# Kernel tuning notes

Measured on AMD Instinct MI355X. Metric: run time of the kernel, lower is better.

The kernel has to match this reference:

```python
import jax, jax.numpy as jnp
import numpy as np

B, S, D = 1, 2048, 4096
HQ, HK, HD = 32, 8, 128


def setup_inputs() -> dict:
    key = jax.random.key(0)
    ks = jax.random.split(key, 6)
    x = jax.random.normal(ks[0], (B, S, D), jnp.float32) * 0.02
    wq = jax.random.normal(ks[1], (D, HQ * HD), jnp.float32) * 0.02
    wk = jax.random.normal(ks[2], (D, HK * HD), jnp.float32) * 0.02
    wv = jax.random.normal(ks[3], (D, HK * HD), jnp.float32) * 0.02
    wo = jax.random.normal(ks[4], (HQ * HD, D), jnp.float32) * 0.02
    # canonical RoPE frequencies: theta = 10000
    inv_freq = 1.0 / (10000.0 ** (jnp.arange(0, HD, 2, dtype=jnp.float32) / HD))  # [HD/2]
    t = jnp.arange(S, dtype=jnp.float32)
    ang = jnp.outer(t, inv_freq)  # [S, HD/2]
    return {
        "x": x,
        "freqs_cos": jnp.cos(ang),
        "freqs_sin": jnp.sin(ang),
        "wq": wq, "wk": wk, "wv": wv, "wo": wo,
    }


def _rope(t, cos, sin):
    # t: [B, S, H, HD]; pairs are consecutive elements (view_as_complex semantics)
    tr = t.reshape(*t.shape[:-1], HD // 2, 2)
    t0, t1 = tr[..., 0], tr[..., 1]
    c = cos[None, :, None, :]
    s = sin[None, :, None, :]
    o0 = t0 * c - t1 * s
    o1 = t0 * s + t1 * c
    return jnp.stack([o0, o1], axis=-1).reshape(t.shape)


def reference(x, freqs_cos, freqs_sin, wq, wk, wv, wo):
    b, s, _ = x.shape
    g = HQ // HK  # GQA group size
    xq = (x @ wq).reshape(b, s, HQ, HD)
    xk = (x @ wk).reshape(b, s, HK, HD)
    xv = (x @ wv).reshape(b, s, HK, HD)
    xq = _rope(xq, freqs_cos, freqs_sin)
    xk = _rope(xk, freqs_cos, freqs_sin)
    scale = 1.0 / jnp.sqrt(jnp.float32(HD))
    xqg = xq.reshape(b, s, HK, g, HD)
    # scores: [b, HK, g, s_q, s_k]
    scores = jnp.einsum("bqkgd,bnkd->bkgqn", xqg, xk) * scale
    causal = jnp.tril(jnp.ones((s, s), dtype=bool))
    scores = jnp.where(causal[None, None, None, :, :], scores, -jnp.inf)
    p = jax.nn.softmax(scores, axis=-1)
    out = jnp.einsum("bkgqn,bnkd->bqkgd", p, xv).reshape(b, s, HQ * HD)
    return out @ wo
```

## Files before the change

### kernel.cpp

```cpp
#include <hip/hip_runtime.h>
#include <stdint.h>

typedef __bf16 bf16_t;
typedef bf16_t bf16x8 __attribute__((ext_vector_type(8)));
typedef float f32x4 __attribute__((ext_vector_type(4)));
typedef unsigned int u32;
typedef unsigned short u16;

#define DEV_INLINE __device__ __forceinline__

#define S_LEN 2048
#define D_MODEL 4096
#define HQ 32
#define HK 8
#define HD 128
#define NQKV 6144

DEV_INLINE u16 f2bf(float x) {
  union { float f; uint32_t u; } v; v.f = x;
  uint32_t r = v.u + 0x7FFFu + ((v.u >> 16) & 1u);
  return (u16)(r >> 16);
}
DEV_INLINE float bf2f(u16 x) {
  union { uint32_t u; float f; } v; v.u = ((uint32_t)x) << 16;
  return v.f;
}
DEV_INLINE u32 pack2bf(float a, float b) {
  return (u32)f2bf(a) | ((u32)f2bf(b) << 16);
}

DEV_INLINE void async_load16(const void* g, void* l) {
  __builtin_amdgcn_global_load_lds(
      (const __attribute__((address_space(1))) u32*)g,
      (__attribute__((address_space(3))) u32*)l, 16, 0, 0);
}

DEV_INLINE f32x4 mfma16(bf16x8 a, bf16x8 b, f32x4 c) {
  return __builtin_amdgcn_mfma_f32_16x16x32_bf16(a, b, c, 0, 0, 0);
}

__global__ void cvt_f32_bf16(const float* __restrict__ in, u16* __restrict__ out, int n) {
  int i = (blockIdx.x * blockDim.x + threadIdx.x) * 4;
  if (i >= n) return;
  float4 v = *(const float4*)(in + i);
  union { u16 s[4]; uint2 u; } o;
  o.s[0] = f2bf(v.x); o.s[1] = f2bf(v.y); o.s[2] = f2bf(v.z); o.s[3] = f2bf(v.w);
  *(uint2*)(out + i) = o.u;
}

__global__ void transpose_f32_bf16(const float* __restrict__ in, u16* __restrict__ out,
                                   int R, int C) {
  __shared__ float tile[32][33];
  int tx = threadIdx.x, ty = threadIdx.y;
  int c0 = blockIdx.x * 32, r0 = blockIdx.y * 32;
#pragma unroll
  for (int i = 0; i < 4; ++i)
    tile[ty + i * 8][tx] = in[(long)(r0 + ty + i * 8) * C + c0 + tx];
  __syncthreads();
#pragma unroll
  for (int i = 0; i < 4; ++i)
    out[(long)(c0 + ty + i * 8) * R + r0 + tx] = f2bf(tile[tx][ty + i * 8]);
}

__global__ void transpose_bf16(const u16* __restrict__ in, u16* __restrict__ out,
                               int R, int C, int ld_in, int col_off) {
  __shared__ u16 tile[32][33];
  int tx = threadIdx.x, ty = threadIdx.y;
  int c0 = blockIdx.x * 32, r0 = blockIdx.y * 32;
#pragma unroll
  for (int i = 0; i < 4; ++i)
    tile[ty + i * 8][tx] = in[(long)(r0 + ty + i * 8) * ld_in + col_off + c0 + tx];
  __syncthreads();
#pragma unroll
  for (int i = 0; i < 4; ++i)
    out[(long)(c0 + ty + i * 8) * R + r0 + tx] = tile[tx][ty + i * 8];
}

__global__ void rope_bf16(const u16* __restrict__ in, const float* __restrict__ cosb,
                          const float* __restrict__ sinb, u16* __restrict__ out,
                          int H, int ld_in, int col_off, float scale) {
  int idx = blockIdx.x * blockDim.x + threadIdx.x;
  int j = idx & 63;
  int sh = idx >> 6;
  int s = sh / H, h = sh - s * H;
  const u16* ip = in + (long)s * ld_in + col_off + h * HD;
  union { u32 u; u16 s2[2]; } v; v.u = *(const u32*)(ip + 2 * j);
  float q0 = bf2f(v.s2[0]), q1 = bf2f(v.s2[1]);
  float c = cosb[s * 64 + j], sn = sinb[s * 64 + j];
  union { u16 s2[2]; u32 u; } o;
  o.s2[0] = f2bf((q0 * c - q1 * sn) * scale);
  o.s2[1] = f2bf((q0 * sn + q1 * c) * scale);
  *(u32*)(out + (long)sh * HD + 2 * j) = o.u;
}

#define BARRIER() asm volatile("s_barrier" ::: "memory")
#define WAIT_VM(N) asm volatile("s_waitcnt vmcnt(" #N ")" ::: "memory")

#define K_TILE(T, DO_STAGE, VMWAIT)                                               \
  {                                                                               \
    const u16* Ab_ = &lds[(T) & 3][0];                                            \
    const u16* Bb_ = &lds[(T) & 3][8192];                                         \
    bf16x8 bfr_[NF];                                                              \
    _Pragma("unroll")                                                             \
    for (int j = 0; j < NF; ++j) bfr_[j] = rdfrag(Bb_, wc * WCOLS + j * 16 + l15);\
    bf16x8 af0_[MFH];                                                             \
    _Pragma("unroll")                                                             \
    for (int i = 0; i < MFH; ++i) af0_[i] = rdfrag(Ab_, wr * MROWS + i * 16 + l15);\
    if (DO_STAGE) stageA((T) + 3);                                                \
    __builtin_amdgcn_s_setprio(1);                                                \
    _Pragma("unroll")                                                             \
    for (int i = 0; i < MFH; ++i)                                                 \
      _Pragma("unroll")                                                           \
      for (int j = 0; j < NF; ++j) acc[i][j] = mfma16(af0_[i], bfr_[j], acc[i][j]);\
    __builtin_amdgcn_s_setprio(0);                                                \
    bf16x8 af1_[MFH];                                                             \
    _Pragma("unroll")                                                             \
    for (int i = 0; i < MFH; ++i)                                                 \
      af1_[i] = rdfrag(Ab_, wr * MROWS + (MFH + i) * 16 + l15);                   \
    if (DO_STAGE) stageB((T) + 3);                                                \
    __builtin_amdgcn_s_setprio(1);                                                \
    _Pragma("unroll")                                                             \
    for (int i = 0; i < MFH; ++i)                                                 \
      _Pragma("unroll")                                                           \
      for (int j = 0; j < NF; ++j)                                                \
        acc[MFH + i][j] = mfma16(af1_[i], bfr_[j], acc[MFH + i][j]);              \
    __builtin_amdgcn_s_setprio(0);                                                \
    VMWAIT;                                                                       \
    BARRIER();                                                                    \
  }

template <int BN, int WM, bool BF16OUT>
__global__ __launch_bounds__(512, 2) void gemm_pipe(
    const u16* __restrict__ A, const u16* __restrict__ Bt, void* __restrict__ Cv,
    int N, int K) {
  constexpr int WN = 8 / WM;
  constexpr int MROWS = 256 / WM;
  constexpr int MF = MROWS / 16;
  constexpr int MFH = MF / 2;
  constexpr int NF = BN / (WN * 16);
  constexpr int WCOLS = NF * 16;
  constexpr int BCH = BN * 4;
  constexpr int BISS = (BCH + 511) / 512;
  constexpr int LDSU = (256 + BN) * 32;

  __shared__ __attribute__((aligned(16))) u16 lds[4][LDSU];

  const int tid = threadIdx.x;
  const int lane = tid & 63;
  const int wave = tid >> 6;
  const int quad = lane >> 4, l15 = lane & 15;
  const int wr = wave / WN, wc = wave % WN;

  const int gx = gridDim.x;
  const int bid = blockIdx.y * gx + blockIdx.x;
  const int cpx = (gx * gridDim.y) >> 3;
  const int sw = (bid & 7) * cpx + (bid >> 3);
  const int bn = sw % gx, bm = sw / gx;

  const long arow = (long)bm * 256, brow = (long)bn * BN;
  const int NT = K >> 5;

  auto stageA = [&](int ts) {
    const int bs = ts & 3;
    const int k0 = ts * 32;
#pragma unroll
    for (int j = 0; j < 2; ++j) {
      int c = tid + j * 512;
      int row = c >> 2, cc = c & 3, cs = cc ^ ((row >> 1) & 3);
      async_load16(A + (arow + row) * (long)K + k0 + cs * 8,
                   (u16*)&lds[bs][0] + c * 8);
    }
  };
  auto stageB = [&](int ts) {
    const int bs = ts & 3;
    const int k0 = ts * 32;
#pragma unroll
    for (int j = 0; j < BISS; ++j) {
      int c = tid + j * 512;
      int cd = (c < BCH) ? c : c - 256;
      int row = cd >> 2, cc = cd & 3, cs = cc ^ ((row >> 1) & 3);
      async_load16(Bt + (brow + row) * (long)K + k0 + cs * 8,
                   (u16*)&lds[bs][8192] + cd * 8);
    }
  };
  auto rdfrag = [&](const u16* base, int row) -> bf16x8 {
    return *(const bf16x8*)(base + row * 32 + ((quad ^ ((row >> 1) & 3)) * 8));
  };

  f32x4 acc[MF][NF] = {};

  stageA(0); stageB(0); stageA(1); stageB(1); stageA(2); stageB(2);
  if constexpr (BISS == 2) { WAIT_VM(8); } else { WAIT_VM(6); }
  BARRIER();

  int t = 0;
  for (; t < NT - 3; ++t) {
    if constexpr (BISS == 2) { K_TILE(t, true, WAIT_VM(8)); }
    else                     { K_TILE(t, true, WAIT_VM(6)); }
  }
  if constexpr (BISS == 2) { K_TILE(t, false, WAIT_VM(4)); }
  else                     { K_TILE(t, false, WAIT_VM(3)); }
  ++t;
  K_TILE(t, false, WAIT_VM(0));
  ++t;
  K_TILE(t, false, ((void)0));

#pragma unroll
  for (int i = 0; i < MF; ++i) {
    const long row = (long)bm * 256 + wr * MROWS + i * 16 + quad * 4;
#pragma unroll
    for (int j = 0; j < NF; ++j) {
      const int col = bn * BN + wc * WCOLS + j * 16 + l15;
      if constexpr (BF16OUT) {
        u16* C = (u16*)Cv;
#pragma unroll
        for (int r = 0; r < 4; ++r) C[(row + r) * N + col] = f2bf(acc[i][j][r]);
      } else {
        float* C = (float*)Cv;
#pragma unroll
        for (int r = 0; r < 4; ++r) C[(row + r) * N + col] = acc[i][j][r];
      }
    }
  }
}

#define NEG_INF -1e30f
__global__ __launch_bounds__(256, 2) void attn_fwd(
    const u16* __restrict__ Qb, const u16* __restrict__ Kb,
    const u16* __restrict__ Vt, u16* __restrict__ Ob) {
  __shared__ __attribute__((aligned(16))) u16 Ks[2][64 * 128];
  __shared__ __attribute__((aligned(16))) u16 Vs[2][128 * 64];
  __shared__ __attribute__((aligned(16))) u16 Pts[4][16 * 64];
  const int tid = threadIdx.x;
  const int lane = tid & 63, wave = tid >> 6;
  const int quad = lane >> 4, l15 = lane & 15;
  const int lin = blockIdx.y * gridDim.x + blockIdx.x;
  const int h = lin & 31;
  const int pp = (lin >> 5) & 7;
  const int u = (lin >> 8) ? 15 - pp : pp;
  const int hk = h >> 2;
  const int swz = 2 * (l15 & 7);
  const int nt = 2 * (u + 1);

  bf16x8 qf[2][4];
#pragma unroll
  for (int n = 0; n < 2; ++n) {
    const u16* qrow = Qb + (long)(u * 128 + wave * 32 + n * 16 + l15) * (HQ * HD)
                      + h * HD + quad * 8;
#pragma unroll
    for (int ks = 0; ks < 4; ++ks) qf[n][ks] = *(const bf16x8*)(qrow + ks * 32);
  }

  auto stage = [&](int t) {
    const int b = t & 1;
#pragma unroll
    for (int it = 0; it < 4; ++it) {
      int c = tid + it * 256;
      int row = c >> 4, cc = c & 15, cs = cc ^ (row & 15);
      async_load16(Kb + (long)(t * 64 + row) * (HK * HD) + hk * HD + cs * 8,
                   (u16*)&Ks[b][0] + c * 8);
    }
#pragma unroll
    for (int it = 0; it < 4; ++it) {
      int c = tid + it * 256;
      int row = c >> 3, cc = c & 7, cs = cc ^ (row & 7);
      async_load16(Vt + (long)(hk * HD + row) * S_LEN + t * 64 + cs * 8,
                   (u16*)&Vs[b][0] + c * 8);
    }
  };

  float m_run[2] = {NEG_INF, NEG_INF}, l_run[2] = {0.f, 0.f};
  f32x4 oacc[8][2] = {};

  stage(0);
  __syncthreads();

  for (int t = 0; t < nt; ++t) {
    const int cur = t & 1;
    if (t + 1 < nt) stage(t + 1);

    if (t * 64 <= u * 128 + wave * 32 + 31) {
      f32x4 sc[4][2] = {};
      __builtin_amdgcn_s_setprio(1);
#pragma unroll
      for (int ks = 0; ks < 4; ++ks)
#pragma unroll
        for (int tj = 0; tj < 4; ++tj) {
          int row = tj * 16 + l15;
          bf16x8 kf = *(const bf16x8*)(&Ks[cur][0] + row * 128
                                       + (((ks * 4 + quad) ^ (row & 15)) * 8));
          sc[tj][0] = mfma16(kf, qf[0][ks], sc[tj][0]);
          sc[tj][1] = mfma16(kf, qf[1][ks], sc[tj][1]);
        }
      __builtin_amdgcn_s_setprio(0);

      const bool diag = (t >= 2 * u);
      const int kbase = t * 64 - u * 128;
#pragma unroll
      for (int n = 0; n < 2; ++n) {
        int qloc = wave * 32 + n * 16 + l15;
        if (diag) {
#pragma unroll
          for (int tj = 0; tj < 4; ++tj)
#pragma unroll
            for (int r = 0; r < 4; ++r)
              if (kbase + tj * 16 + quad * 4 + r > qloc) sc[tj][n][r] = NEG_INF;
        }
        float m = NEG_INF;
#pragma unroll
        for (int tj = 0; tj < 4; ++tj)
#pragma unroll
          for (int r = 0; r < 4; ++r) m = fmaxf(m, sc[tj][n][r]);
        m = fmaxf(m, __shfl_xor(m, 16));
        m = fmaxf(m, __shfl_xor(m, 32));
        if (!__all(m - m_run[n] <= 8.0f)) {
          float mnew = fmaxf(m_run[n], m);
          float alpha = __expf(m_run[n] - mnew);
          m_run[n] = mnew;
          l_run[n] *= alpha;
#pragma unroll
          for (int tj = 0; tj < 8; ++tj) oacc[tj][n] *= alpha;
        }
        float rs = 0.f;
#pragma unroll
        for (int tj = 0; tj < 4; ++tj)
#pragma unroll
          for (int r = 0; r < 4; ++r) {
            float p = __expf(sc[tj][n][r] - m_run[n]);
            sc[tj][n][r] = p;
            rs += p;
          }
        rs += __shfl_xor(rs, 16);
        rs += __shfl_xor(rs, 32);
        l_run[n] += rs;
      }

      u16* pw = &Pts[wave][0];
      bf16x8 pf0[2], pf1[2];
#pragma unroll
      for (int tj = 0; tj < 4; ++tj) {
        union { u32 w[2]; uint2 u2; } pk;
        pk.w[0] = pack2bf(sc[tj][0][0], sc[tj][0][1]);
        pk.w[1] = pack2bf(sc[tj][0][2], sc[tj][0][3]);
        *(uint2*)(pw + l15 * 64 + (((tj * 4 + quad) ^ swz) * 4)) = pk.u2;
      }
      __asm__ volatile("s_waitcnt lgkmcnt(0)" ::: "memory");
#pragma unroll
      for (int ks = 0; ks < 2; ++ks)
        pf0[ks] = *(const bf16x8*)(pw + l15 * 64 + (((ks * 8 + quad * 2) ^ swz) * 4));
      __asm__ volatile("s_waitcnt lgkmcnt(0)" ::: "memory");
#pragma unroll
      for (int tj = 0; tj < 4; ++tj) {
        union { u32 w[2]; uint2 u2; } pk;
        pk.w[0] = pack2bf(sc[tj][1][0], sc[tj][1][1]);
        pk.w[1] = pack2bf(sc[tj][1][2], sc[tj][1][3]);
        *(uint2*)(pw + l15 * 64 + (((tj * 4 + quad) ^ swz) * 4)) = pk.u2;
      }
      __asm__ volatile("s_waitcnt lgkmcnt(0)" ::: "memory");
#pragma unroll
      for (int ks = 0; ks < 2; ++ks)
        pf1[ks] = *(const bf16x8*)(pw + l15 * 64 + (((ks * 8 + quad * 2) ^ swz) * 4));

      __builtin_amdgcn_s_setprio(1);
#pragma unroll
      for (int ks = 0; ks < 2; ++ks)
#pragma unroll
        for (int tj = 0; tj < 8; ++tj) {
          int row = tj * 16 + l15;
          bf16x8 vf = *(const bf16x8*)(&Vs[cur][0] + row * 64
                                       + (((ks * 4 + quad) ^ (row & 7)) * 8));
          oacc[tj][0] = mfma16(vf, pf0[ks], oacc[tj][0]);
          oacc[tj][1] = mfma16(vf, pf1[ks], oacc[tj][1]);
        }
      __builtin_amdgcn_s_setprio(0);
    }

    __syncthreads();
  }

#pragma unroll
  for (int n = 0; n < 2; ++n) {
    float inv_l = 1.0f / l_run[n];
    long grow = u * 128 + wave * 32 + n * 16 + l15;
#pragma unroll
    for (int tj = 0; tj < 8; ++tj) {
      int gcol = h * HD + tj * 16 + quad * 4;
      union { u32 w[2]; uint2 u2; } pk;
      pk.w[0] = pack2bf(oacc[tj][n][0] * inv_l, oacc[tj][n][1] * inv_l);
      pk.w[1] = pack2bf(oacc[tj][n][2] * inv_l, oacc[tj][n][3] * inv_l);
      *(uint2*)(Ob + grow * (HQ * HD) + gcol) = pk.u2;
    }
  }
}

#define MB (1024L * 1024L)

extern "C" void kernel_launch(void* const* d_in, const int* in_sizes, int n_in,
                              void* d_out, int out_size, void* d_ws, size_t ws_size,
                              hipStream_t stream) {
  const float* x    = (const float*)d_in[0];
  const float* fcos = (const float*)d_in[1];
  const float* fsin = (const float*)d_in[2];
  const float* wq   = (const float*)d_in[3];
  const float* wk   = (const float*)d_in[4];
  const float* wv   = (const float*)d_in[5];
  const float* wo   = (const float*)d_in[6];
  float* out = (float*)d_out;

  char* ws = (char*)d_ws;
  u16* wt    = (u16*)(ws + 0 * MB);
  u16* xb    = (u16*)(ws + 48 * MB);
  u16* QKVb  = (u16*)(ws + 64 * MB);
  u16* Qb    = (u16*)(ws + 88 * MB);
  u16* Kb    = (u16*)(ws + 104 * MB);
  u16* Vt    = (u16*)(ws + 108 * MB);
  u16* attnb = (u16*)(ws + 112 * MB);

  const int M = S_LEN, D = D_MODEL;

  cvt_f32_bf16<<<(M * D) / 1024, 256, 0, stream>>>(x, xb, M * D);

  transpose_f32_bf16<<<dim3(D / 32, D / 32), dim3(32, 8), 0, stream>>>(wq, wt, D, HQ * HD);
  transpose_f32_bf16<<<dim3((HK * HD) / 32, D / 32), dim3(32, 8), 0, stream>>>(
      wk, wt + (long)(HQ * HD) * D, D, HK * HD);
  transpose_f32_bf16<<<dim3((HK * HD) / 32, D / 32), dim3(32, 8), 0, stream>>>(
      wv, wt + (long)(HQ * HD + HK * HD) * D, D, HK * HD);

  gemm_pipe<192, 2, true><<<dim3(NQKV / 192, M / 256), 512, 0, stream>>>(
      xb, wt, QKVb, NQKV, D);

  rope_bf16<<<(M * HQ * 64) / 256, 256, 0, stream>>>(
      QKVb, fcos, fsin, Qb, HQ, NQKV, 0, 0.08838834764831845f);
  rope_bf16<<<(M * HK * 64) / 256, 256, 0, stream>>>(
      QKVb, fcos, fsin, Kb, HK, NQKV, HQ * HD, 1.0f);
  transpose_bf16<<<dim3((HK * HD) / 32, M / 32), dim3(32, 8), 0, stream>>>(
      QKVb, Vt, M, HK * HD, NQKV, HQ * HD + HK * HD);

  attn_fwd<<<dim3(16, HQ), 256, 0, stream>>>(Qb, Kb, Vt, attnb);

  transpose_f32_bf16<<<dim3(D / 32, D / 32), dim3(32, 8), 0, stream>>>(wo, wt, HQ * HD, D);
  gemm_pipe<128, 4, false><<<dim3(D / 128, M / 256), 512, 0, stream>>>(
      attnb, wt, out, D, HQ * HD);
}
```

Before: 478.3 us.

## Replace LDS-staged GEMM with B-direct-to-register variant on smaller M tiles

Rewrites both projection GEMMs so that only the A tile (128 rows) is staged through LDS with async loads, while each wave loads its own B columns straight from global memory into registers with one-tile-ahead double buffering. Block size drops from 512 to 256 threads, the M tile drops from 256 to 128, and each wave covers all rows for a slice of columns. The aim is to cut LDS traffic and footprint for B and to simplify synchronisation. The cost is uncoalesced per-lane B global loads, no reuse of B across waves through LDS, and a loop that only waits on a barrier with no explicit vmcnt wait.

```diff
diff --git a/kernel.cpp b/kernel.cpp
--- a/kernel.cpp
+++ b/kernel.cpp
@@ -96,60 +96,16 @@
 #define BARRIER() asm volatile("s_barrier" ::: "memory")
 #define WAIT_VM(N) asm volatile("s_waitcnt vmcnt(" #N ")" ::: "memory")
 
-#define K_TILE(T, DO_STAGE, VMWAIT)                                               \
-  {                                                                               \
-    const u16* Ab_ = &lds[(T) & 3][0];                                            \
-    const u16* Bb_ = &lds[(T) & 3][8192];                                         \
-    bf16x8 bfr_[NF];                                                              \
-    _Pragma("unroll")                                                             \
-    for (int j = 0; j < NF; ++j) bfr_[j] = rdfrag(Bb_, wc * WCOLS + j * 16 + l15);\
-    bf16x8 af0_[MFH];                                                             \
-    _Pragma("unroll")                                                             \
-    for (int i = 0; i < MFH; ++i) af0_[i] = rdfrag(Ab_, wr * MROWS + i * 16 + l15);\
-    if (DO_STAGE) stageA((T) + 3);                                                \
-    __builtin_amdgcn_s_setprio(1);                                                \
-    _Pragma("unroll")                                                             \
-    for (int i = 0; i < MFH; ++i)                                                 \
-      _Pragma("unroll")                                                           \
-      for (int j = 0; j < NF; ++j) acc[i][j] = mfma16(af0_[i], bfr_[j], acc[i][j]);\
-    __builtin_amdgcn_s_setprio(0);                                                \
-    bf16x8 af1_[MFH];                                                             \
-    _Pragma("unroll")                                                             \
-    for (int i = 0; i < MFH; ++i)                                                 \
-      af1_[i] = rdfrag(Ab_, wr * MROWS + (MFH + i) * 16 + l15);                   \
-    if (DO_STAGE) stageB((T) + 3);                                                \
-    __builtin_amdgcn_s_setprio(1);                                                \
-    _Pragma("unroll")                                                             \
-    for (int i = 0; i < MFH; ++i)                                                 \
-      _Pragma("unroll")                                                           \
-      for (int j = 0; j < NF; ++j)                                                \
-        acc[MFH + i][j] = mfma16(af1_[i], bfr_[j], acc[MFH + i][j]);              \
-    __builtin_amdgcn_s_setprio(0);                                                \
-    VMWAIT;                                                                       \
-    BARRIER();                                                                    \
-  }
-
-template <int BN, int WM, bool BF16OUT>
-__global__ __launch_bounds__(512, 2) void gemm_pipe(
+template <int BN, bool BF16OUT>
+__global__ __launch_bounds__(256, 2) void gemm_bdir(
     const u16* __restrict__ A, const u16* __restrict__ Bt, void* __restrict__ Cv,
     int N, int K) {
-  constexpr int WN = 8 / WM;
-  constexpr int MROWS = 256 / WM;
-  constexpr int MF = MROWS / 16;
-  constexpr int MFH = MF / 2;
-  constexpr int NF = BN / (WN * 16);
-  constexpr int WCOLS = NF * 16;
-  constexpr int BCH = BN * 4;
-  constexpr int BISS = (BCH + 511) / 512;
-  constexpr int LDSU = (256 + BN) * 32;
-
-  __shared__ __attribute__((aligned(16))) u16 lds[4][LDSU];
+  constexpr int NF = BN / 64;
+  __shared__ __attribute__((aligned(16))) u16 lds[4][128 * 32];
 
   const int tid = threadIdx.x;
-  const int lane = tid & 63;
-  const int wave = tid >> 6;
+  const int lane = tid & 63, wave = tid >> 6;
   const int quad = lane >> 4, l15 = lane & 15;
-  const int wr = wave / WN, wc = wave % WN;
 
   const int gx = gridDim.x;
   const int bid = blockIdx.y * gx + blockIdx.x;
@@ -157,60 +113,74 @@
   const int sw = (bid & 7) * cpx + (bid >> 3);
   const int bn = sw % gx, bm = sw / gx;
 
-  const long arow = (long)bm * 256, brow = (long)bn * BN;
+  const long arow = (long)bm * 128, brow = (long)bn * BN;
   const int NT = K >> 5;
 
+  const u16* asrc[2];
+  int adst[2];
+#pragma unroll
+  for (int j = 0; j < 2; ++j) {
+    int c = tid + j * 256;
+    int row = c >> 2, cc = c & 3, cs = cc ^ ((row >> 1) & 3);
+    asrc[j] = A + (arow + row) * (long)K + cs * 8;
+    adst[j] = c * 8;
+  }
+  const u16* bptr[NF];
+#pragma unroll
+  for (int j = 0; j < NF; ++j)
+    bptr[j] = Bt + (brow + wave * (NF * 16) + j * 16 + l15) * (long)K + quad * 8;
+
   auto stageA = [&](int ts) {
-    const int bs = ts & 3;
     const int k0 = ts * 32;
-#pragma unroll
-    for (int j = 0; j < 2; ++j) {
-      int c = tid + j * 512;
-      int row = c >> 2, cc = c & 3, cs = cc ^ ((row >> 1) & 3);
-      async_load16(A + (arow + row) * (long)K + k0 + cs * 8,
-                   (u16*)&lds[bs][0] + c * 8);
-    }
+    u16* base = &lds[ts & 3][0];
+#pragma unroll
+    for (int j = 0; j < 2; ++j) async_load16(asrc[j] + k0, base + adst[j]);
   };
-  auto stageB = [&](int ts) {
-    const int bs = ts & 3;
-    const int k0 = ts * 32;
-#pragma unroll
-    for (int j = 0; j < BISS; ++j) {
-      int c = tid + j * 512;
-      int cd = (c < BCH) ? c : c - 256;
-      int row = cd >> 2, cc = cd & 3, cs = cc ^ ((row >> 1) & 3);
-      async_load16(Bt + (brow + row) * (long)K + k0 + cs * 8,
-                   (u16*)&lds[bs][8192] + cd * 8);
-    }
-  };
-  auto rdfrag = [&](const u16* base, int row) -> bf16x8 {
-    return *(const bf16x8*)(base + row * 32 + ((quad ^ ((row >> 1) & 3)) * 8));
-  };
-
-  f32x4 acc[MF][NF] = {};
-
-  stageA(0); stageB(0); stageA(1); stageB(1); stageA(2); stageB(2);
-  if constexpr (BISS == 2) { WAIT_VM(8); } else { WAIT_VM(6); }
+
+  f32x4 acc[8][NF] = {};
+  bf16x8 b0[NF], b1[NF];
+
+  stageA(0); stageA(1); stageA(2);
+#pragma unroll
+  for (int j = 0; j < NF; ++j) b0[j] = *(const bf16x8*)(bptr[j]);
+  WAIT_VM(0);
   BARRIER();
 
-  int t = 0;
-  for (; t < NT - 3; ++t) {
-    if constexpr (BISS == 2) { K_TILE(t, true, WAIT_VM(8)); }
-    else                     { K_TILE(t, true, WAIT_VM(6)); }
-  }
-  if constexpr (BISS == 2) { K_TILE(t, false, WAIT_VM(4)); }
-  else                     { K_TILE(t, false, WAIT_VM(3)); }
-  ++t;
-  K_TILE(t, false, WAIT_VM(0));
-  ++t;
-  K_TILE(t, false, ((void)0));
-
-#pragma unroll
-  for (int i = 0; i < MF; ++i) {
-    const long row = (long)bm * 256 + wr * MROWS + i * 16 + quad * 4;
+#define GD_TILE(T, BR, BPRE)                                             \
+  {                                                                      \
+    if ((T) + 3 < NT) stageA((T) + 3);                                   \
+    if ((T) + 1 < NT) {                                                  \
+      _Pragma("unroll")                                                  \
+      for (int j = 0; j < NF; ++j)                                       \
+        BPRE[j] = *(const bf16x8*)(bptr[j] + ((T) + 1) * 32);            \
+    }                                                                    \
+    const u16* lbase = &lds[(T) & 3][0];                                 \
+    __builtin_amdgcn_s_setprio(1);                                       \
+    _Pragma("unroll")                                                    \
+    for (int i = 0; i < 8; ++i) {                                        \
+      int row = i * 16 + l15;                                            \
+      bf16x8 af = *(const bf16x8*)(lbase + row * 32 +                    \
+                                   ((quad ^ ((row >> 1) & 3)) * 8));     \
+      _Pragma("unroll")                                                  \
+      for (int j = 0; j < NF; ++j)                                       \
+        acc[i][j] = mfma16(af, BR[j], acc[i][j]);                        \
+    }                                                                    \
+    __builtin_amdgcn_s_setprio(0);                                       \
+    BARRIER();                                                           \
+  }
+
+  for (int t = 0; t < NT; t += 2) {
+    GD_TILE(t, b0, b1);
+    GD_TILE(t + 1, b1, b0);
+  }
+#undef GD_TILE
+
+#pragma unroll
+  for (int i = 0; i < 8; ++i) {
+    const long row = (long)bm * 128 + i * 16 + quad * 4;
 #pragma unroll
     for (int j = 0; j < NF; ++j) {
-      const int col = bn * BN + wc * WCOLS + j * 16 + l15;
+      const int col = bn * BN + wave * (NF * 16) + j * 16 + l15;
       if constexpr (BF16OUT) {
         u16* C = (u16*)Cv;
 #pragma unroll
@@ -426,7 +396,7 @@
   transpose_f32_bf16<<<dim3((HK * HD) / 32, D / 32), dim3(32, 8), 0, stream>>>(
       wv, wt + (long)(HQ * HD + HK * HD) * D, D, HK * HD);
 
-  gemm_pipe<192, 2, true><<<dim3(NQKV / 192, M / 256), 512, 0, stream>>>(
+  gemm_bdir<192, true><<<dim3(NQKV / 192, M / 128), 256, 0, stream>>>(
       xb, wt, QKVb, NQKV, D);
 
   rope_bf16<<<(M * HQ * 64) / 256, 256, 0, stream>>>(
@@ -439,6 +409,6 @@
   attn_fwd<<<dim3(16, HQ), 256, 0, stream>>>(Qb, Kb, Vt, attnb);
 
   transpose_f32_bf16<<<dim3(D / 32, D / 32), dim3(32, 8), 0, stream>>>(wo, wt, HQ * HD, D);
-  gemm_pipe<128, 4, false><<<dim3(D / 128, M / 256), 512, 0, stream>>>(
+  gemm_bdir<128, false><<<dim3(D / 128, M / 128), 256, 0, stream>>>(
       attnb, wt, out, D, HQ * HD);
 }
```

After: 548.6 us. 1.15x slower.
